# Kernel tuning notes

Measured on AMD Instinct MI355X. Metric: run time of the kernel, lower is better.

Reference implementation:

```python
import jax, jax.numpy as jnp
import numpy as np

V = 8192
E = 262144
IN_DIM = 128
OUT_DIM = 128
NEG_SLOPE = 0.2


def setup_inputs() -> dict:
    key = jax.random.key(0)
    k1, k2, k3, k4 = jax.random.split(key, 4)
    h = jax.random.normal(k1, (V, IN_DIM), dtype=jnp.float32)
    edge_index = jax.random.randint(k2, (2, E), 0, V, dtype=jnp.int64)
    # nn.Linear weights: W (out_dim, in_dim), att (1, 2*out_dim), both bias-free
    W = jax.random.normal(k3, (OUT_DIM, IN_DIM), dtype=jnp.float32) / np.sqrt(IN_DIM)
    att_w = jax.random.normal(k4, (1, 2 * OUT_DIM), dtype=jnp.float32) / np.sqrt(2 * OUT_DIM)
    return {"h": h, "edge_index": edge_index, "W": W, "att_w": att_w}


def reference(h, edge_index, W, att_w):
    # h: (V, in_dim) -> (V, out_dim)
    hw = h @ W.T
    src, dst = edge_index[0], edge_index[1]
    # edge features: concat of endpoint embeddings -> (E, 2*out_dim)
    e = jnp.concatenate([hw[src], hw[dst]], axis=-1)
    # attention logits per edge, LeakyReLU(0.2)
    a = jax.nn.leaky_relu(jnp.squeeze(e @ att_w.T, -1), negative_slope=NEG_SLOPE)
    v = hw.shape[0]
    # faithful to original: dense V x V matrix, zeros on non-edges,
    # softmax over ALL columns (non-edges included as score 0)
    alpha = jnp.zeros((v, v), dtype=hw.dtype).at[src, dst].set(a)
    alpha = jax.nn.softmax(alpha, axis=-1)
    # dropout is identity in eval mode (deterministic reference)
    return alpha @ hw
```

## Files before the change

### kernel.cpp

```cpp
#include <hip/hip_runtime.h>
#include <hip/hip_bf16.h>
#include <math.h>


#define V 8192
#define E 262144
#define D 128
#define NEG_SLOPE 0.2f
#define CAP 96

#define FMA4(acc, hv, wv) { acc.x += (hv)*(wv).x; acc.y += (hv)*(wv).y; \
                            acc.z += (hv)*(wv).z; acc.w += (hv)*(wv).w; }

__device__ __forceinline__ unsigned short f2bf(float f) {
    unsigned u = __float_as_uint(f);
    return (unsigned short)((u + 0x7fffu + ((u >> 16) & 1u)) >> 16);
}
__device__ __forceinline__ float bf2f_low(int p) {
    return __uint_as_float(((unsigned)p) << 16);
}

__global__ __launch_bounds__(256) void k_hw(const float* __restrict__ h,
                                            const float* __restrict__ W,
                                            const float* __restrict__ att,
                                            unsigned short* __restrict__ hwb,
                                            float* __restrict__ s1,
                                            float* __restrict__ s2,
                                            float* __restrict__ Pb,
                                            int* __restrict__ cnt) {
    __shared__ float Wt[D * 132];
    __shared__ float atts[2 * D];
    __shared__ float scr[8 * D];
    int t = threadIdx.x, b = blockIdx.x;
    if (b < 32) cnt[b * 256 + t] = 0;
    atts[t] = att[t];
    for (int f4 = t; f4 < (D * D) / 4; f4 += 256) {
        int o = f4 >> 5, k = (f4 & 31) * 4;
        float4 wv = *(const float4*)&W[o * D + k];
        Wt[(k + 0) * 132 + o] = wv.x;
        Wt[(k + 1) * 132 + o] = wv.y;
        Wt[(k + 2) * 132 + o] = wv.z;
        Wt[(k + 3) * 132 + o] = wv.w;
    }
    __syncthreads();

    int c4 = (t & 31) * 4;
    int rq = t >> 5;
    int r0 = b * 32;
    float4 a0 = make_float4(0.f,0.f,0.f,0.f), a1 = a0, a2 = a0, a3 = a0;
    const float* h0p = &h[(r0 + rq     ) * D];
    const float* h1p = &h[(r0 + rq +  8) * D];
    const float* h2p = &h[(r0 + rq + 16) * D];
    const float* h3p = &h[(r0 + rq + 24) * D];
    #pragma unroll 4
    for (int kq = 0; kq < D; kq += 4) {
        float4 w0 = *(const float4*)&Wt[(kq + 0) * 132 + c4];
        float4 w1 = *(const float4*)&Wt[(kq + 1) * 132 + c4];
        float4 w2 = *(const float4*)&Wt[(kq + 2) * 132 + c4];
        float4 w3 = *(const float4*)&Wt[(kq + 3) * 132 + c4];
        float4 hv;
        hv = *(const float4*)&h0p[kq];
        FMA4(a0, hv.x, w0); FMA4(a0, hv.y, w1); FMA4(a0, hv.z, w2); FMA4(a0, hv.w, w3);
        hv = *(const float4*)&h1p[kq];
        FMA4(a1, hv.x, w0); FMA4(a1, hv.y, w1); FMA4(a1, hv.z, w2); FMA4(a1, hv.w, w3);
        hv = *(const float4*)&h2p[kq];
        FMA4(a2, hv.x, w0); FMA4(a2, hv.y, w1); FMA4(a2, hv.z, w2); FMA4(a2, hv.w, w3);
        hv = *(const float4*)&h3p[kq];
        FMA4(a3, hv.x, w0); FMA4(a3, hv.y, w1); FMA4(a3, hv.z, w2); FMA4(a3, hv.w, w3);
    }
    *(ushort4*)&hwb[(r0 + rq     ) * D + c4] = make_ushort4(f2bf(a0.x), f2bf(a0.y), f2bf(a0.z), f2bf(a0.w));
    *(ushort4*)&hwb[(r0 + rq +  8) * D + c4] = make_ushort4(f2bf(a1.x), f2bf(a1.y), f2bf(a1.z), f2bf(a1.w));
    *(ushort4*)&hwb[(r0 + rq + 16) * D + c4] = make_ushort4(f2bf(a2.x), f2bf(a2.y), f2bf(a2.z), f2bf(a2.w));
    *(ushort4*)&hwb[(r0 + rq + 24) * D + c4] = make_ushort4(f2bf(a3.x), f2bf(a3.y), f2bf(a3.z), f2bf(a3.w));

    float q1[4], q2[4];
    float4* accs[4] = {&a0, &a1, &a2, &a3};
    #pragma unroll
    for (int r = 0; r < 4; ++r) {
        float4 v = *accs[r];
        q1[r] = v.x * atts[c4] + v.y * atts[c4 + 1] + v.z * atts[c4 + 2] + v.w * atts[c4 + 3];
        q2[r] = v.x * atts[D + c4] + v.y * atts[D + c4 + 1] + v.z * atts[D + c4 + 2] + v.w * atts[D + c4 + 3];
    }
    #pragma unroll
    for (int m = 16; m; m >>= 1) {
        #pragma unroll
        for (int r = 0; r < 4; ++r) {
            q1[r] += __shfl_xor(q1[r], m);
            q2[r] += __shfl_xor(q2[r], m);
        }
    }
    if ((t & 31) == 0) {
        #pragma unroll
        for (int r = 0; r < 4; ++r) {
            s1[r0 + rq + r * 8] = q1[r];
            s2[r0 + rq + r * 8] = q2[r];
        }
    }

    scr[rq * D + c4 + 0] = a0.x + a1.x + a2.x + a3.x;
    scr[rq * D + c4 + 1] = a0.y + a1.y + a2.y + a3.y;
    scr[rq * D + c4 + 2] = a0.z + a1.z + a2.z + a3.z;
    scr[rq * D + c4 + 3] = a0.w + a1.w + a2.w + a3.w;
    __syncthreads();
    if (t < D) {
        float s = 0.f;
        #pragma unroll
        for (int r = 0; r < 8; ++r) s += scr[r * D + t];
        Pb[b * D + t] = s;
    }
}

__global__ __launch_bounds__(256) void k_scatter(const int* __restrict__ ei,
                                                 const float* __restrict__ s1,
                                                 const float* __restrict__ s2,
                                                 int* __restrict__ cnt,
                                                 int* __restrict__ bucket,
                                                 const float* __restrict__ Pb,
                                                 float* __restrict__ S) {
    int b = blockIdx.x, t = threadIdx.x;
    if (b < 1024) {
        int g = b * 256 + t;
        int src = ei[g];
        int dst = ei[E + g];
        float a = s1[src] + s2[dst];
        a = a > 0.f ? a : NEG_SLOPE * a;
        float w = expf(a) - 1.f;
        int pos = atomicAdd(&cnt[src], 1);
        if (pos < CAP)
            bucket[src * CAP + pos] = (dst << 16) | (int)f2bf(w);
    } else {
        __shared__ float red[256];
        int c = t & 127, half = t >> 7;
        float s = 0.f;
        #pragma unroll 4
        for (int r = half; r < 256; r += 2)
            s += Pb[r * D + c];
        red[t] = s;
        __syncthreads();
        if (t < D) S[t] = red[t] + red[D + t];
    }
}

__global__ __launch_bounds__(256) void k_row(const int* __restrict__ bucket,
                                             const int* __restrict__ cnt,
                                             const unsigned short* __restrict__ hwb,
                                             const float* __restrict__ S,
                                             float* __restrict__ out) {
    __shared__ int lb[4][CAP];
    int t = threadIdx.x;
    int wv = t >> 6, lane = t & 63;
    int row = blockIdx.x * 4 + wv;
    int deg = cnt[row];
    if (deg > CAP) deg = CAP;
    const int* bk = bucket + row * CAP;
    int e0 = bk[lane];
    int e1 = (lane < CAP - 64) ? bk[64 + lane] : 0;
    int p0 = (lane < deg)      ? e0 : (int)0xFFFF0000;
    int p1 = (64 + lane < deg) ? e1 : (int)0xFFFF0000;
    lb[wv][lane] = p0;
    if (lane < CAP - 64) lb[wv][64 + lane] = p1;
    int d0 = p0 >> 16;
    int d1 = p1 >> 16;
    int n0 = deg < 64 ? deg : 64;
    float accx = 0.f, accy = 0.f, dex = 0.f;
    const int* myb = lb[wv];
    int col2 = lane * 2;
    int j = 0;
    for (; j + 4 <= n0; j += 4) {
        int4 pq = *(const int4*)&myb[j];
        int dj0 = pq.x >> 16, dj1 = pq.y >> 16, dj2 = pq.z >> 16, dj3 = pq.w >> 16;
        unsigned hv0 = *(const unsigned*)&hwb[dj0 * D + col2];
        unsigned hv1 = *(const unsigned*)&hwb[dj1 * D + col2];
        unsigned hv2 = *(const unsigned*)&hwb[dj2 * D + col2];
        unsigned hv3 = *(const unsigned*)&hwb[dj3 * D + col2];
        unsigned long long m0 = __ballot(d0 == dj0);
        unsigned long long m1 = __ballot(d0 == dj1);
        unsigned long long m2 = __ballot(d0 == dj2);
        unsigned long long m3 = __ballot(d0 == dj3);
        float w0 = (m0 & ((1ull << (j + 0)) - 1ull)) ? 0.f : bf2f_low(pq.x);
        float w1 = (m1 & ((1ull << (j + 1)) - 1ull)) ? 0.f : bf2f_low(pq.y);
        float w2 = (m2 & ((1ull << (j + 2)) - 1ull)) ? 0.f : bf2f_low(pq.z);
        float w3 = (m3 & ((1ull << (j + 3)) - 1ull)) ? 0.f : bf2f_low(pq.w);
        accx += w0 * __uint_as_float(hv0 << 16);
        accy += w0 * __uint_as_float(hv0 & 0xFFFF0000u);
        accx += w1 * __uint_as_float(hv1 << 16);
        accy += w1 * __uint_as_float(hv1 & 0xFFFF0000u);
        accx += w2 * __uint_as_float(hv2 << 16);
        accy += w2 * __uint_as_float(hv2 & 0xFFFF0000u);
        accx += w3 * __uint_as_float(hv3 << 16);
        accy += w3 * __uint_as_float(hv3 & 0xFFFF0000u);
        dex += w0 + w1 + w2 + w3;
    }
    for (; j < n0; ++j) {
        int pj = myb[j];
        int dj = pj >> 16;
        float wj = bf2f_low(pj);
        unsigned long long m = __ballot(d0 == dj);
        if (m & ((1ull << j) - 1ull)) wj = 0.f;
        unsigned hv = *(const unsigned*)&hwb[dj * D + col2];
        accx += wj * __uint_as_float(hv << 16);
        accy += wj * __uint_as_float(hv & 0xFFFF0000u);
        dex += wj;
    }
    for (j = 64; j < deg; ++j) {
        int pj = myb[j];
        int dj = pj >> 16;
        float wj = bf2f_low(pj);
        unsigned long long m0 = __ballot(d0 == dj);
        unsigned long long m1 = __ballot(d1 == dj) & ((1ull << (j - 64)) - 1ull);
        if (m0 | m1) wj = 0.f;
        unsigned hv = *(const unsigned*)&hwb[dj * D + col2];
        accx += wj * __uint_as_float(hv << 16);
        accy += wj * __uint_as_float(hv & 0xFFFF0000u);
        dex += wj;
    }
    float inv = 1.f / ((float)V + dex);
    float2 s = *(const float2*)&S[col2];
    float2 o;
    o.x = (s.x + accx) * inv;
    o.y = (s.y + accy) * inv;
    *(float2*)&out[row * D + col2] = o;
}

extern "C" void kernel_launch(void* const* d_in, const int* in_sizes, int n_in,
                              void* d_out, int out_size, void* d_ws, size_t ws_size,
                              hipStream_t stream) {
    const float* h   = (const float*)d_in[0];
    const int*   ei  = (const int*)d_in[1];
    const float* W   = (const float*)d_in[2];
    const float* att = (const float*)d_in[3];
    float* out = (float*)d_out;

    char* ws = (char*)d_ws;
    unsigned short* hwb = (unsigned short*)(ws);
    float* s1  = (float*)(ws + 2097152);
    float* s2  = (float*)(ws + 2129920);
    float* S   = (float*)(ws + 2162688);
    int*   cnt = (int*)(ws + 2163200);
    int*   bucket = (int*)(ws + 2195968);
    float* Pb  = (float*)(ws + 5341696);

    k_hw     <<<256,  256, 0, stream>>>(h, W, att, hwb, s1, s2, Pb, cnt);
    k_scatter<<<1025, 256, 0, stream>>>(ei, s1, s2, cnt, bucket, Pb, S);
    k_row    <<<2048, 256, 0, stream>>>(bucket, cnt, hwb, S, out);
}
```

Baseline: 106.0 us.

## Compute attention scores via W^T·att and overlap GEMM with edge scatter

Precomputes u = W^T·att so per-node attention scores s1/s2 come straight from h in a light first kernel, and column sums of h are multiplied by W to get S. The dense h·W GEMM moves into the second kernel, where it runs alongside the edge-scatter blocks, taking it off the critical path ahead of the scatter. This costs a small redundant per-block W^T·att computation and a serial 256-row reduction plus a matvec in one block.

```diff
diff --git a/kernel.cpp b/kernel.cpp
--- a/kernel.cpp
+++ b/kernel.cpp
@@ -20,106 +20,104 @@
     return __uint_as_float(((unsigned)p) << 16);
 }
 
-__global__ __launch_bounds__(256) void k_hw(const float* __restrict__ h,
-                                            const float* __restrict__ W,
-                                            const float* __restrict__ att,
-                                            unsigned short* __restrict__ hwb,
-                                            float* __restrict__ s1,
-                                            float* __restrict__ s2,
-                                            float* __restrict__ Pb,
-                                            int* __restrict__ cnt) {
-    __shared__ float Wt[D * 132];
+__global__ __launch_bounds__(256) void k_pre(const float* __restrict__ h,
+                                             const float* __restrict__ W,
+                                             const float* __restrict__ att,
+                                             float* __restrict__ s1,
+                                             float* __restrict__ s2,
+                                             float* __restrict__ Pc,
+                                             int* __restrict__ cnt) {
     __shared__ float atts[2 * D];
-    __shared__ float scr[8 * D];
+    __shared__ float us[2 * D];
+    __shared__ float csc[4][D];
     int t = threadIdx.x, b = blockIdx.x;
+    atts[t] = att[t];
     if (b < 32) cnt[b * 256 + t] = 0;
-    atts[t] = att[t];
-    for (int f4 = t; f4 < (D * D) / 4; f4 += 256) {
-        int o = f4 >> 5, k = (f4 & 31) * 4;
-        float4 wv = *(const float4*)&W[o * D + k];
-        Wt[(k + 0) * 132 + o] = wv.x;
-        Wt[(k + 1) * 132 + o] = wv.y;
-        Wt[(k + 2) * 132 + o] = wv.z;
-        Wt[(k + 3) * 132 + o] = wv.w;
-    }
-    __syncthreads();
-
-    int c4 = (t & 31) * 4;
-    int rq = t >> 5;
-    int r0 = b * 32;
-    float4 a0 = make_float4(0.f,0.f,0.f,0.f), a1 = a0, a2 = a0, a3 = a0;
-    const float* h0p = &h[(r0 + rq     ) * D];
-    const float* h1p = &h[(r0 + rq +  8) * D];
-    const float* h2p = &h[(r0 + rq + 16) * D];
-    const float* h3p = &h[(r0 + rq + 24) * D];
-    #pragma unroll 4
-    for (int kq = 0; kq < D; kq += 4) {
-        float4 w0 = *(const float4*)&Wt[(kq + 0) * 132 + c4];
-        float4 w1 = *(const float4*)&Wt[(kq + 1) * 132 + c4];
-        float4 w2 = *(const float4*)&Wt[(kq + 2) * 132 + c4];
-        float4 w3 = *(const float4*)&Wt[(kq + 3) * 132 + c4];
-        float4 hv;
-        hv = *(const float4*)&h0p[kq];
-        FMA4(a0, hv.x, w0); FMA4(a0, hv.y, w1); FMA4(a0, hv.z, w2); FMA4(a0, hv.w, w3);
-        hv = *(const float4*)&h1p[kq];
-        FMA4(a1, hv.x, w0); FMA4(a1, hv.y, w1); FMA4(a1, hv.z, w2); FMA4(a1, hv.w, w3);
-        hv = *(const float4*)&h2p[kq];
-        FMA4(a2, hv.x, w0); FMA4(a2, hv.y, w1); FMA4(a2, hv.z, w2); FMA4(a2, hv.w, w3);
-        hv = *(const float4*)&h3p[kq];
-        FMA4(a3, hv.x, w0); FMA4(a3, hv.y, w1); FMA4(a3, hv.z, w2); FMA4(a3, hv.w, w3);
-    }
-    *(ushort4*)&hwb[(r0 + rq     ) * D + c4] = make_ushort4(f2bf(a0.x), f2bf(a0.y), f2bf(a0.z), f2bf(a0.w));
-    *(ushort4*)&hwb[(r0 + rq +  8) * D + c4] = make_ushort4(f2bf(a1.x), f2bf(a1.y), f2bf(a1.z), f2bf(a1.w));
-    *(ushort4*)&hwb[(r0 + rq + 16) * D + c4] = make_ushort4(f2bf(a2.x), f2bf(a2.y), f2bf(a2.z), f2bf(a2.w));
-    *(ushort4*)&hwb[(r0 + rq + 24) * D + c4] = make_ushort4(f2bf(a3.x), f2bf(a3.y), f2bf(a3.z), f2bf(a3.w));
-
-    float q1[4], q2[4];
-    float4* accs[4] = {&a0, &a1, &a2, &a3};
-    #pragma unroll
-    for (int r = 0; r < 4; ++r) {
-        float4 v = *accs[r];
-        q1[r] = v.x * atts[c4] + v.y * atts[c4 + 1] + v.z * atts[c4 + 2] + v.w * atts[c4 + 3];
-        q2[r] = v.x * atts[D + c4] + v.y * atts[D + c4 + 1] + v.z * atts[D + c4 + 2] + v.w * atts[D + c4 + 3];
-    }
-    #pragma unroll
-    for (int m = 16; m; m >>= 1) {
-        #pragma unroll
-        for (int r = 0; r < 4; ++r) {
-            q1[r] += __shfl_xor(q1[r], m);
-            q2[r] += __shfl_xor(q2[r], m);
-        }
-    }
-    if ((t & 31) == 0) {
-        #pragma unroll
-        for (int r = 0; r < 4; ++r) {
-            s1[r0 + rq + r * 8] = q1[r];
-            s2[r0 + rq + r * 8] = q2[r];
-        }
-    }
-
-    scr[rq * D + c4 + 0] = a0.x + a1.x + a2.x + a3.x;
-    scr[rq * D + c4 + 1] = a0.y + a1.y + a2.y + a3.y;
-    scr[rq * D + c4 + 2] = a0.z + a1.z + a2.z + a3.z;
-    scr[rq * D + c4 + 3] = a0.w + a1.w + a2.w + a3.w;
     __syncthreads();
     if (t < D) {
-        float s = 0.f;
+        float u1 = 0.f, u2 = 0.f;
+        #pragma unroll 8
+        for (int o = 0; o < D; ++o) {
+            float wv = W[o * D + t];
+            u1 += wv * atts[o];
+            u2 += wv * atts[D + o];
+        }
+        us[t] = u1; us[D + t] = u2;
+    }
+    __syncthreads();
+    int wv = t >> 6, lane = t & 63;
+    float2 u1v = *(const float2*)&us[lane * 2];
+    float2 u2v = *(const float2*)&us[D + lane * 2];
+    int r0 = b * 32 + wv * 8;
+    float cx = 0.f, cy = 0.f;
+    #pragma unroll
+    for (int r = 0; r < 8; ++r) {
+        float2 hv = *(const float2*)&h[(r0 + r) * D + lane * 2];
+        cx += hv.x; cy += hv.y;
+        float p1 = hv.x * u1v.x + hv.y * u1v.y;
+        float p2 = hv.x * u2v.x + hv.y * u2v.y;
         #pragma unroll
-        for (int r = 0; r < 8; ++r) s += scr[r * D + t];
-        Pb[b * D + t] = s;
-    }
-}
-
-__global__ __launch_bounds__(256) void k_scatter(const int* __restrict__ ei,
-                                                 const float* __restrict__ s1,
-                                                 const float* __restrict__ s2,
-                                                 int* __restrict__ cnt,
-                                                 int* __restrict__ bucket,
-                                                 const float* __restrict__ Pb,
-                                                 float* __restrict__ S) {
-    int b = blockIdx.x, t = threadIdx.x;
-    if (b < 1024) {
-        int g = b * 256 + t;
+        for (int m = 32; m; m >>= 1) { p1 += __shfl_xor(p1, m); p2 += __shfl_xor(p2, m); }
+        if (lane == 0) { s1[r0 + r] = p1; s2[r0 + r] = p2; }
+    }
+    *(float2*)&csc[wv][lane * 2] = make_float2(cx, cy);
+    __syncthreads();
+    if (t < D)
+        Pc[b * D + t] = csc[0][t] + csc[1][t] + csc[2][t] + csc[3][t];
+}
+
+__global__ __launch_bounds__(256) void k_mid(const float* __restrict__ h,
+                                             const float* __restrict__ W,
+                                             const int* __restrict__ ei,
+                                             const float* __restrict__ s1,
+                                             const float* __restrict__ s2,
+                                             const float* __restrict__ Pc,
+                                             unsigned short* __restrict__ hwb,
+                                             float* __restrict__ S,
+                                             int* __restrict__ cnt,
+                                             int* __restrict__ bucket) {
+    __shared__ float Wt[D * 132];
+    int t = threadIdx.x, b = blockIdx.x;
+    if (b < 256) {
+        for (int f4 = t; f4 < (D * D) / 4; f4 += 256) {
+            int o = f4 >> 5, k = (f4 & 31) * 4;
+            float4 wv = *(const float4*)&W[o * D + k];
+            Wt[(k + 0) * 132 + o] = wv.x;
+            Wt[(k + 1) * 132 + o] = wv.y;
+            Wt[(k + 2) * 132 + o] = wv.z;
+            Wt[(k + 3) * 132 + o] = wv.w;
+        }
+        __syncthreads();
+        int c4 = (t & 31) * 4;
+        int rq = t >> 5;
+        int r0 = b * 32;
+        float4 a0 = make_float4(0.f,0.f,0.f,0.f), a1 = a0, a2 = a0, a3 = a0;
+        const float* h0p = &h[(r0 + rq     ) * D];
+        const float* h1p = &h[(r0 + rq +  8) * D];
+        const float* h2p = &h[(r0 + rq + 16) * D];
+        const float* h3p = &h[(r0 + rq + 24) * D];
+        #pragma unroll 4
+        for (int kq = 0; kq < D; kq += 4) {
+            float4 w0 = *(const float4*)&Wt[(kq + 0) * 132 + c4];
+            float4 w1 = *(const float4*)&Wt[(kq + 1) * 132 + c4];
+            float4 w2 = *(const float4*)&Wt[(kq + 2) * 132 + c4];
+            float4 w3 = *(const float4*)&Wt[(kq + 3) * 132 + c4];
+            float4 hv;
+            hv = *(const float4*)&h0p[kq];
+            FMA4(a0, hv.x, w0); FMA4(a0, hv.y, w1); FMA4(a0, hv.z, w2); FMA4(a0, hv.w, w3);
+            hv = *(const float4*)&h1p[kq];
+            FMA4(a1, hv.x, w0); FMA4(a1, hv.y, w1); FMA4(a1, hv.z, w2); FMA4(a1, hv.w, w3);
+            hv = *(const float4*)&h2p[kq];
+            FMA4(a2, hv.x, w0); FMA4(a2, hv.y, w1); FMA4(a2, hv.z, w2); FMA4(a2, hv.w, w3);
+            hv = *(const float4*)&h3p[kq];
+            FMA4(a3, hv.x, w0); FMA4(a3, hv.y, w1); FMA4(a3, hv.z, w2); FMA4(a3, hv.w, w3);
+        }
+        *(ushort4*)&hwb[(r0 + rq     ) * D + c4] = make_ushort4(f2bf(a0.x), f2bf(a0.y), f2bf(a0.z), f2bf(a0.w));
+        *(ushort4*)&hwb[(r0 + rq +  8) * D + c4] = make_ushort4(f2bf(a1.x), f2bf(a1.y), f2bf(a1.z), f2bf(a1.w));
+        *(ushort4*)&hwb[(r0 + rq + 16) * D + c4] = make_ushort4(f2bf(a2.x), f2bf(a2.y), f2bf(a2.z), f2bf(a2.w));
+        *(ushort4*)&hwb[(r0 + rq + 24) * D + c4] = make_ushort4(f2bf(a3.x), f2bf(a3.y), f2bf(a3.z), f2bf(a3.w));
+    } else if (b < 1280) {
+        int g = (b - 256) * 256 + t;
         int src = ei[g];
         int dst = ei[E + g];
         float a = s1[src] + s2[dst];
@@ -129,15 +127,23 @@
         if (pos < CAP)
             bucket[src * CAP + pos] = (dst << 16) | (int)f2bf(w);
     } else {
-        __shared__ float red[256];
-        int c = t & 127, half = t >> 7;
-        float s = 0.f;
-        #pragma unroll 4
-        for (int r = half; r < 256; r += 2)
-            s += Pb[r * D + c];
-        red[t] = s;
+        if (t < D) {
+            float c = 0.f;
+            #pragma unroll 8
+            for (int bb = 0; bb < 256; ++bb) c += Pc[bb * D + t];
+            Wt[t] = c;
+        }
         __syncthreads();
-        if (t < D) S[t] = red[t] + red[D + t];
+        if (t < D) {
+            float acc = 0.f;
+            #pragma unroll
+            for (int k = 0; k < D; k += 4) {
+                float4 wv = *(const float4*)&W[t * D + k];
+                float4 cv = *(const float4*)&Wt[k];
+                acc += wv.x * cv.x + wv.y * cv.y + wv.z * cv.z + wv.w * cv.w;
+            }
+            S[t] = acc;
+        }
     }
 }
 
@@ -238,9 +244,9 @@
     float* S   = (float*)(ws + 2162688);
     int*   cnt = (int*)(ws + 2163200);
     int*   bucket = (int*)(ws + 2195968);
-    float* Pb  = (float*)(ws + 5341696);
-
-    k_hw     <<<256,  256, 0, stream>>>(h, W, att, hwb, s1, s2, Pb, cnt);
-    k_scatter<<<1025, 256, 0, stream>>>(ei, s1, s2, cnt, bucket, Pb, S);
-    k_row    <<<2048, 256, 0, stream>>>(bucket, cnt, hwb, S, out);
-}
+    float* Pc  = (float*)(ws + 5341696);
+
+    k_pre<<<256,  256, 0, stream>>>(h, W, att, s1, s2, Pc, cnt);
+    k_mid<<<1281, 256, 0, stream>>>(h, W, ei, s1, s2, Pc, hwb, S, cnt, bucket);
+    k_row<<<2048, 256, 0, stream>>>(bucket, cnt, hwb, S, out);
+}
```

Measured after the change: 106.9 us. About the same (+0.8%).
